# Performance work log

Measured on AMD Instinct MI355X. Metric: run time of the kernel, lower is better.

Reference implementation:

```python
import jax, jax.numpy as jnp
import numpy as np

N, B, NPM = 16384, 256, 64          # nodes, molecules, nodes per molecule
E = 65536                           # edges
FMAX, AMAX = 32, 16                 # FG slots per molecule, atoms per FG
HID, FGE, POSE = 960, 512, 128
NFG, MAXTOK, NFEAT = 205, 160, 5


def setup_inputs() -> dict:
    key = jax.random.key(0)
    ks = jax.random.split(key, 12)
    graph_x = jax.random.normal(ks[0], (N, NFEAT), jnp.float32)
    edge_index = jax.random.randint(ks[1], (2, E), 0, N)
    graph_batch = jnp.arange(N) // NPM
    ptr = jnp.arange(B + 1) * NPM
    fg_type_tensor = jax.random.randint(ks[2], (B, FMAX), 0, NFG)
    idx = jax.random.randint(ks[3], (B, FMAX, AMAX), 0, NPM)
    drop = jax.random.uniform(ks[4], (B, FMAX, AMAX)) < 0.3
    fg_indices_tensor = jnp.where(drop, -1, idx)
    s = lambda k, sh: jax.random.normal(k, sh, jnp.float32) * 0.02
    return dict(
        graph_x=graph_x, edge_index=edge_index, graph_batch=graph_batch, ptr=ptr,
        fg_type_tensor=fg_type_tensor, fg_indices_tensor=fg_indices_tensor,
        W1=s(ks[5], (NFEAT, HID)), b1=jnp.zeros((HID,), jnp.float32),
        W2=s(ks[6], (HID, HID)), b2=jnp.zeros((HID,), jnp.float32),
        fg_embed=s(ks[7], (NFG, FGE)), pos_embed=s(ks[8], (MAXTOK, POSE)),
        projW=s(ks[9], (HID, HID)), projb=jnp.zeros((HID,), jnp.float32),
        fuseW=s(ks[10], (FGE + POSE + HID + HID, HID)), fuseb=jnp.zeros((HID,), jnp.float32),
    )


def gcn_conv(x, W, b, src, dst, n):
    # PyG GCNConv: linear, add self-loops, symmetric deg^-1/2 normalization, sum-aggregate, bias
    h = x @ W
    deg = 1.0 + jax.ops.segment_sum(jnp.ones(src.shape[0], h.dtype), dst, num_segments=n)
    dinv = jax.lax.rsqrt(deg)
    msg = h[src] * (dinv[src] * dinv[dst])[:, None]            # [E, HID]
    out = jax.ops.segment_sum(msg, dst, num_segments=n) + h * (dinv * dinv)[:, None]
    return out + b


def reference(graph_x, edge_index, graph_batch, ptr, fg_type_tensor, fg_indices_tensor,
              W1, b1, W2, b2, fg_embed, pos_embed, projW, projb, fuseW, fuseb):
    src, dst = edge_index[0], edge_index[1]
    n = graph_x.shape[0]
    h = jax.nn.relu(gcn_conv(graph_x, W1, b1, src, dst, n))
    h = gcn_conv(h, W2, b2, src, dst, n)

    Bsz, Fmax = fg_type_tensor.shape
    # global mean pool per molecule
    cnt = jax.ops.segment_sum(jnp.ones(n, h.dtype), graph_batch, num_segments=Bsz)
    global_emb = jax.ops.segment_sum(h, graph_batch, num_segments=Bsz) / cnt[:, None]

    fg_static = fg_embed[fg_type_tensor]                        # [B, F, FGE]
    fg_pos = jnp.broadcast_to(pos_embed[:Fmax][None], (Bsz, Fmax, pos_embed.shape[1]))

    # vectorized FG-specific node pooling (replaces nested python loops)
    mask = fg_indices_tensor >= 0                               # [B, F, A]
    gids = jnp.where(mask, ptr[:-1][:, None, None] + fg_indices_tensor, 0)
    gathered = h[gids] * mask[..., None].astype(h.dtype)        # [B, F, A, HID]
    counts = mask.sum(-1).astype(h.dtype)                       # [B, F]
    pooled = gathered.sum(-2) / jnp.maximum(counts, 1.0)[..., None]
    fg_valid_mask = counts > 0

    fg_node_proj = pooled @ projW + projb
    global_exp = jnp.broadcast_to(global_emb[:, None, :], (Bsz, Fmax, global_emb.shape[1]))
    fused = jnp.concatenate([fg_static, fg_pos, fg_node_proj, global_exp], axis=-1)
    fg_fused = fused @ fuseW + fuseb
    return fg_fused, fg_valid_mask
```

## Files before the change

kernel.cpp:

```cpp
#include <hip/hip_runtime.h>

typedef unsigned short u16;
typedef unsigned int u32;
typedef __attribute__((ext_vector_type(8))) short short8;
typedef __attribute__((ext_vector_type(4))) float f32x4;

#define N_NODES 16384
#define B_MOL   256
#define NPM     64
#define E_EDGES 65536
#define FMAXF   32
#define AMAXA   16
#define HID     960
#define NFG     205
#define BF_ROWS 8192
#define OUT1    7864320
#define NTOT    4516800

__device__ __forceinline__ float bf2f(u16 u){ u32 x=((u32)u)<<16; float f; __builtin_memcpy(&f,&x,4); return f; }
__device__ __forceinline__ u16 f2bf(float f){ u32 x; __builtin_memcpy(&x,&f,4); x += 0x7FFFu + ((x>>16)&1u); return (u16)(x>>16); }

__device__ __forceinline__ void gload_lds16(const u16* g, u16* l){
    __builtin_amdgcn_global_load_lds(
        (const __attribute__((address_space(1))) void*)g,
        (__attribute__((address_space(3))) void*)l, 16, 0, 0);
}
__device__ __forceinline__ size_t swzA(int row, int col){
    return ((size_t)((row>>4)*30 + (col>>5)))*512 + (size_t)(((((col>>3)&3)*16) + (row&15))*8);
}
__device__ __forceinline__ size_t swzE(int row, int col){
    return ((size_t)((row>>4)*30 + (col>>5)))*512 + (size_t)((((col>>3)&3)*16 + (row&15))*8 + (col&7));
}

struct NormSrcs { const void* p[11]; };
__global__ __launch_bounds__(256) void k_normAll(NormSrcs s, u16* __restrict__ region,
                                                 float* __restrict__ b2f, float* __restrict__ projbf,
                                                 float* __restrict__ z4, int* __restrict__ flag,
                                                 int* __restrict__ deg){
    __shared__ int cnt;
    int t = threadIdx.x;
    if (t==0) cnt = 0;
    __syncthreads();
    u16 pv = ((const u16*)s.p[0])[t*2];
    if (((pv>>7)&0xFF) >= 0xC0) atomicAdd(&cnt, 1);
    __syncthreads();
    int fl = (cnt > 16) ? 1 : 0;
    int i = blockIdx.x*256 + t;
    if (blockIdx.x==0 && t==0) *flag = fl;
    if (i < N_NODES) deg[i] = 0;
    if (i < 4*HID) z4[i] = 0.f;
    if (i >= NTOT) return;
    int seg, off;
    if      (i <   81920){seg=0;  off=i;}
    else if (i <   86720){seg=1;  off=i-81920;}
    else if (i <   87680){seg=2;  off=i-86720;}
    else if (i < 1009280){seg=3;  off=i-87680;}
    else if (i < 1010240){seg=4;  off=i-1009280;}
    else if (i < 1115200){seg=5;  off=i-1010240;}
    else if (i < 1135680){seg=6;  off=i-1115200;}
    else if (i < 2057280){seg=7;  off=i-1135680;}
    else if (i < 2058240){seg=8;  off=i-2057280;}
    else if (i < 4515840){seg=9;  off=i-2058240;}
    else                 {seg=10; off=i-4515840;}
    const void* sp = s.p[seg];
    float fv; u16 uv;
    if (fl){ fv = ((const float*)sp)[off]; uv = f2bf(fv); }
    else   { uv = ((const u16*)sp)[off];  fv = bf2f(uv); }
    region[i] = uv;
    if (seg==4) b2f[off] = fv;
    if (seg==8) projbf[off] = fv;
}


__device__ __forceinline__ void gemm_sq(int bx, int by, const u16* __restrict__ A, int lda,
                                        const u16* __restrict__ Bt, int ldb,
                                        u16* __restrict__ C, int swz, char* smem)
{
    u16* As = (u16*)smem;
    u16* Bs = (u16*)smem + 64*40;
    const int tid = threadIdx.x;
    const int wave = tid>>6, lane = tid&63;
    const int wm = wave>>1, wn = wave&1;
    const int q = lane>>4, l16 = lane&15;
    const int m0 = bx*64, n0 = by*64;
    const int sm = tid>>2, sk = (tid&3)*8;
    f32x4 acc00={0,0,0,0}, acc01={0,0,0,0}, acc10={0,0,0,0}, acc11={0,0,0,0};
    const u16* Ap = A + (size_t)(m0+sm)*lda + sk;
    const u16* Bp = Bt + (size_t)(n0+sm)*ldb + sk;
    for (int k0=0; k0<HID; k0+=32){
        short8 av = *(const short8*)(Ap + k0);
        short8 bv = *(const short8*)(Bp + k0);
        *(short8*)(As + sm*40 + sk) = av;
        *(short8*)(Bs + sm*40 + sk) = bv;
        __syncthreads();
        short8 a0 = *(const short8*)(As + (wm*32      + l16)*40 + q*8);
        short8 a1 = *(const short8*)(As + (wm*32 + 16 + l16)*40 + q*8);
        short8 b0 = *(const short8*)(Bs + (wn*32      + l16)*40 + q*8);
        short8 b1 = *(const short8*)(Bs + (wn*32 + 16 + l16)*40 + q*8);
        acc00 = __builtin_amdgcn_mfma_f32_16x16x32_bf16(a0,b0,acc00,0,0,0);
        acc01 = __builtin_amdgcn_mfma_f32_16x16x32_bf16(a0,b1,acc01,0,0,0);
        acc10 = __builtin_amdgcn_mfma_f32_16x16x32_bf16(a1,b0,acc10,0,0,0);
        acc11 = __builtin_amdgcn_mfma_f32_16x16x32_bf16(a1,b1,acc11,0,0,0);
        __syncthreads();
    }
    #pragma unroll
    for (int i=0;i<2;i++){
        int rowb = m0 + wm*32 + i*16 + q*4;
        #pragma unroll
        for (int j=0;j<2;j++){
            int col = n0 + wn*32 + j*16 + l16;
            f32x4 av = (i==0) ? ((j==0)?acc00:acc01) : ((j==0)?acc10:acc11);
            #pragma unroll
            for (int r=0;r<4;r++){
                int row = rowb + r;
                u16 o = f2bf(av[r]);
                if (swz) C[swzE(row,col)] = o;
                else     C[(size_t)row*HID + col] = o;
            }
        }
    }
}
__device__ __forceinline__ void gemm64f(int bx, int by, const u16* __restrict__ A, int lda,
                                        const u16* __restrict__ Bt, int ldb,
                                        float* __restrict__ C, int M, int K,
                                        const float* __restrict__ addv, char* smem)
{
    u16* As = (u16*)smem;
    u16* Bs = (u16*)smem + 64*40;
    const int tid = threadIdx.x;
    const int wave = tid>>6, lane = tid&63;
    const int wm = wave>>1, wn = wave&1;
    const int q = lane>>4, l16 = lane&15;
    const int m0 = bx*64, n0 = by*64;
    const int sm = tid>>2, sk = (tid&3)*8;
    f32x4 acc00={0,0,0,0}, acc01={0,0,0,0}, acc10={0,0,0,0}, acc11={0,0,0,0};
    const bool aOk = (m0+sm) < M;
    const u16* Ap = A + (size_t)(m0+sm)*lda + sk;
    const u16* Bp = Bt + (size_t)(n0+sm)*ldb + sk;
    for (int k0=0; k0<K; k0+=32){
        short8 av = {0,0,0,0,0,0,0,0};
        if (aOk) av = *(const short8*)(Ap + k0);
        short8 bv = *(const short8*)(Bp + k0);
        *(short8*)(As + sm*40 + sk) = av;
        *(short8*)(Bs + sm*40 + sk) = bv;
        __syncthreads();
        short8 a0 = *(const short8*)(As + (wm*32      + l16)*40 + q*8);
        short8 a1 = *(const short8*)(As + (wm*32 + 16 + l16)*40 + q*8);
        short8 b0 = *(const short8*)(Bs + (wn*32      + l16)*40 + q*8);
        short8 b1 = *(const short8*)(Bs + (wn*32 + 16 + l16)*40 + q*8);
        acc00 = __builtin_amdgcn_mfma_f32_16x16x32_bf16(a0,b0,acc00,0,0,0);
        acc01 = __builtin_amdgcn_mfma_f32_16x16x32_bf16(a0,b1,acc01,0,0,0);
        acc10 = __builtin_amdgcn_mfma_f32_16x16x32_bf16(a1,b0,acc10,0,0,0);
        acc11 = __builtin_amdgcn_mfma_f32_16x16x32_bf16(a1,b1,acc11,0,0,0);
        __syncthreads();
    }
    #pragma unroll
    for (int i=0;i<2;i++){
        int rowb = m0 + wm*32 + i*16 + q*4;
        #pragma unroll
        for (int j=0;j<2;j++){
            int col = n0 + wn*32 + j*16 + l16;
            f32x4 av = (i==0) ? ((j==0)?acc00:acc01) : ((j==0)?acc10:acc11);
            float add = addv ? addv[col] : 0.f;
            #pragma unroll
            for (int r=0;r<4;r++){
                int row = rowb + r;
                if (row < M) C[(size_t)row*HID + col] = av[r] + add;
            }
        }
    }
}
__device__ __forceinline__ void transpose_tile(int bx, int by, const u16* __restrict__ src,
                                               u16* __restrict__ dst, int R, int C, char* smem)
{
    u16 (*tl)[33] = (u16(*)[33])smem;
    int c0 = bx*32, r0 = by*32;
    int tx = threadIdx.x & 31, ty = threadIdx.x >> 5;
    #pragma unroll
    for (int i=0;i<4;i++) tl[ty+i*8][tx] = src[(size_t)(r0+ty+i*8)*C + c0+tx];
    __syncthreads();
    #pragma unroll
    for (int i=0;i<4;i++) dst[(size_t)(c0+ty+i*8)*R + r0+tx] = tl[tx][ty+i*8];
}
__device__ __forceinline__ void vecmat_body(int bx, int by, const float* __restrict__ v,
                                            const u16* __restrict__ M, float* __restrict__ out, char* smem)
{
    float (*part)[64] = (float(*)[64])smem;
    int tid = threadIdx.x;
    int cl = tid & 63;
    int c = bx*64 + cl;
    int kg = tid >> 6;
    int k0 = by*60 + kg*15;
    float s = 0.f;
    #pragma unroll
    for (int i=0;i<15;i++) s += v[k0+i]*bf2f(M[(size_t)(k0+i)*HID + c]);
    part[kg][cl] = s;
    __syncthreads();
    if (kg==0) atomicAdd(&out[c], part[0][cl]+part[1][cl]+part[2][cl]+part[3][cl]);
}
__device__ __forceinline__ void scandinv_body(const int* __restrict__ deg, int* __restrict__ off,
                                              int* __restrict__ cur, float* __restrict__ dinv, char* smem)
{
    int* ps = (int*)smem;
    int t = threadIdx.x;
    const int chunk = N_NODES/256;
    int base0 = t*chunk;
    int s = 0;
    for (int i=0;i<chunk;i++) s += deg[base0+i];
    ps[t] = s; __syncthreads();
    for (int ofs=1; ofs<256; ofs<<=1){
        int v = ps[t];
        int add = (t>=ofs) ? ps[t-ofs] : 0;
        __syncthreads();
        ps[t] = v + add;
        __syncthreads();
    }
    int run = (t==0) ? 0 : ps[t-1];
    for (int i=0;i<chunk;i++){
        int d = deg[base0+i];
        off[base0+i]=run; cur[base0+i]=run; run += d;
        dinv[base0+i] = rsqrtf(1.0f + (float)d);
    }
    if (t==255) off[N_NODES] = run;
}

__global__ __launch_bounds__(256) void k_L1(const u16* __restrict__ fuseWn, u16* __restrict__ fuseWT,
                                            const int* __restrict__ dst, int* __restrict__ deg){
    __shared__ __attribute__((aligned(16))) char smem[2112];
    int b = blockIdx.x;
    if (b < 2400){
        transpose_tile(b%30, b/30, fuseWn, fuseWT, 2560, HID, smem);
    } else {
        int e = (b-2400)*256 + threadIdx.x;
        if (e < E_EDGES) atomicAdd(&deg[dst[e]], 1);
    }
}
__global__ __launch_bounds__(256) void k_L2(const u16* fuseWT, const u16* projWn, const u16* W2n,
                                            u16* Ub, u16* WglobT,
                                            const int* deg, int* off, int* cur, float* dinv){
    __shared__ __attribute__((aligned(16))) char smem[10240];
    int b = blockIdx.x;
    if (b < 450){
        int z = b/225, r = b%225;
        if (z==0) gemm_sq(r%15, r/15, fuseWT+640, 2560, projWn, HID, Ub, 0, smem);
        else      gemm_sq(r%15, r/15, fuseWT+1600, 2560, W2n, HID, WglobT, 0, smem);
    } else {
        scandinv_body(deg, off, cur, dinv, smem);
    }
}
__global__ __launch_bounds__(256) void k_L3(const u16* Ub, const u16* W2n, u16* WbigS,
                                            const u16* fgeN, const u16* posN, const u16* fuseWT,
                                            float* fgA, float* pWbM,
                                            const int* src, const int* dst, const float* dinv,
                                            int* cur, int* csr_s, float* csr_w){
    __shared__ __attribute__((aligned(16))) char smem[10240];
    int b = blockIdx.x;
    if (b < 225){
        gemm_sq(b%15, b/15, Ub, HID, W2n, HID, WbigS, 1, smem);
    } else if (b < 300){
        int bb = b-225;
        if (bb < 60) gemm64f(bb%4, bb/4, fgeN, 512, fuseWT, 2560, fgA, NFG, 512, nullptr, smem);
        else         gemm64f(0, bb-60, posN, 128, fuseWT+512, 2560, pWbM, FMAXF, 128, nullptr, smem);
    } else {
        int e = (b-300)*256 + threadIdx.x;
        if (e < E_EDGES){
            int s = src[e], d = dst[e];
            int p = atomicAdd(&cur[d], 1);
            csr_s[p] = s;
            csr_w[p] = dinv[s]*dinv[d];
        }
    }
}
__global__ __launch_bounds__(256) void k_L4(const u16* __restrict__ gxn, const float* __restrict__ dinv,
                                            const int* __restrict__ off, const int* __restrict__ csr_s,
                                            const float* __restrict__ csr_w,
                                            const u16* __restrict__ W1, const u16* __restrict__ b1,
                                            u16* __restrict__ h1b,
                                            const float* b2f, const float* projbf, const u16* fuseWn,
                                            const u16* projWn, float* tvb, float* cC, float* gvec){
    __shared__ __attribute__((aligned(16))) char smem[1024];
    int b = blockIdx.x;
    if (b < 8192){
        float* a2 = (float*)smem;
        int t = threadIdx.x;
        int h = t>>7, tl = t&127;
        int n = b*2 + h;
        if (tl < 5){
            int k = tl;
            float di = dinv[n], sw = di*di;
            float a = sw * bf2f(gxn[n*5+k]);
            int j0 = off[n], j1 = off[n+1];
            for (int j=j0;j<j1;j++) a += csr_w[j]*bf2f(gxn[csr_s[j]*5+k]);
            a2[h*8+k] = a;
        }
        __syncthreads();
        if (tl < 120){
            int c8 = tl*8;
            float a[5];
            #pragma unroll
            for (int k=0;k<5;k++) a[k] = a2[h*8+k];
            float r[8];
            short8 bb = *(const short8*)(b1 + c8);
            #pragma unroll
            for (int j=0;j<8;j++) r[j] = bf2f(((u16*)&bb)[j]);
            #pragma unroll
            for (int k=0;k<5;k++){
                short8 wv = *(const short8*)(W1 + k*HID + c8);
                #pragma unroll
                for (int j=0;j<8;j++) r[j] += a[k]*bf2f(((u16*)&wv)[j]);
            }
            short8 o;
            #pragma unroll
            for (int j=0;j<8;j++) ((u16*)&o)[j] = f2bf(fmaxf(r[j],0.f));
            *(short8*)(h1b + (size_t)n*HID + c8) = o;
        }
    } else {
        int bb = b - 8192;
        int z = bb/240, r = bb%240;
        if (z==0)      vecmat_body(r%15, r/15, b2f,    projWn,            tvb,  smem);
        else if (z==1) vecmat_body(r%15, r/15, projbf, fuseWn + 640*HID,  cC,   smem);
        else           vecmat_body(r%15, r/15, b2f,    fuseWn + 1600*HID, gvec, smem);
    }
}
__global__ __launch_bounds__(256) void k_L5(const u16* __restrict__ h1b, const float* __restrict__ dinv,
                                            const int* __restrict__ off, const int* __restrict__ csr_s,
                                            const float* __restrict__ csr_w, u16* __restrict__ P1b,
                                            const float* tvb, const u16* fuseWn, float* vb,
                                            const float* cC, const float* gvec, const u16* fusebn, float* c0){
    __shared__ __attribute__((aligned(16))) char smem[1024];
    int b = blockIdx.x;
    if (b < 4096){
        int wv = threadIdx.x>>6, lane = threadIdx.x&63;
        int n = b*4 + wv;
        int c = lane*16;
        bool act = lane < 60;
        float di = dinv[n], sw = di*di;
        float acc[16];
        if (act){
            short8 h0 = *(const short8*)(h1b + (size_t)n*HID + c);
            short8 h1v = *(const short8*)(h1b + (size_t)n*HID + c + 8);
            #pragma unroll
            for (int j=0;j<8;j++){ acc[j] = sw*bf2f(((u16*)&h0)[j]); acc[8+j] = sw*bf2f(((u16*)&h1v)[j]); }
        } else {
            #pragma unroll
            for (int j=0;j<16;j++) acc[j] = 0.f;
        }
        int j0 = off[n], j1 = off[n+1];
        for (int j=j0;j<j1;j++){
            int s = csr_s[j]; float w = csr_w[j];
            if (act){
                short8 v0 = *(const short8*)(h1b + (size_t)s*HID + c);
                short8 v1 = *(const short8*)(h1b + (size_t)s*HID + c + 8);
                #pragma unroll
                for (int j2=0;j2<8;j2++){ acc[j2] += w*bf2f(((u16*)&v0)[j2]); acc[8+j2] += w*bf2f(((u16*)&v1)[j2]); }
            }
        }
        if (act){
            short8 o0, o1;
            #pragma unroll
            for (int j=0;j<8;j++){ ((u16*)&o0)[j] = f2bf(acc[j]); ((u16*)&o1)[j] = f2bf(acc[8+j]); }
            *(short8*)(P1b + (size_t)n*HID + c) = o0;
            *(short8*)(P1b + (size_t)n*HID + c + 8) = o1;
        }
    } else if (b < 4336){
        int bb = b - 4096;
        vecmat_body(bb%15, bb/15, tvb, fuseWn + 640*HID, vb, smem);
    } else {
        int c = (b-4336)*256 + threadIdx.x;
        if (c < HID) c0[c] = cC[c] + gvec[c] + bf2f(fusebn[c]);
    }
}
__global__ __launch_bounds__(256) void k_L6(const u16* __restrict__ P1b, const int* __restrict__ fgi,
                                            const int* __restrict__ ptr, u16* __restrict__ prb,
                                            float* __restrict__ evec, u16* __restrict__ maskb,
                                            float* __restrict__ maskf, const int* __restrict__ flag,
                                            u16* __restrict__ gmb){
    int b = blockIdx.x;
    if (b < 2048){
        int wv = threadIdx.x>>6, lane = threadIdx.x&63;
        int bf = b*4 + wv;
        int mb = bf >> 5;
        int base = ptr[mb];
        int c = lane*16;
        bool act = lane < 60;
        float acc[16];
        #pragma unroll
        for (int j=0;j<16;j++) acc[j] = 0.f;
        int cnt = 0;
        #pragma unroll
        for (int a=0;a<AMAXA;a++){
            int idx = fgi[bf*AMAXA + a];
            if (idx >= 0){
                cnt++;
                if (act){
                    short8 v0 = *(const short8*)(P1b + (size_t)(base+idx)*HID + c);
                    short8 v1 = *(const short8*)(P1b + (size_t)(base+idx)*HID + c + 8);
                    #pragma unroll
                    for (int j=0;j<8;j++){ acc[j] += bf2f(((u16*)&v0)[j]); acc[8+j] += bf2f(((u16*)&v1)[j]); }
                }
            }
        }
        float inv = (cnt>0) ? 1.0f/(float)cnt : 0.0f;
        if (act){
            short8 o0, o1;
            #pragma unroll
            for (int j=0;j<8;j++){ ((u16*)&o0)[j] = f2bf(acc[j]*inv); ((u16*)&o1)[j] = f2bf(acc[8+j]*inv); }
            *(short8*)(prb + swzA(bf, c)) = o0;
            *(short8*)(prb + swzA(bf, c+8)) = o1;
        }
        if (lane == 0){
            float e = (cnt>0) ? 1.0f : 0.0f;
            evec[bf] = e;
            if (*flag) maskf[bf] = e;
            else       maskb[bf] = f2bf(e);
        }
    } else {
        int id = (b-2048)*256 + threadIdx.x;
        int mb = id / 120; int c8 = (id - mb*120)*8;
        float s[8] = {0,0,0,0,0,0,0,0};
        for (int i=0;i<NPM;i++){
            short8 v = *(const short8*)(P1b + (size_t)(mb*NPM+i)*HID + c8);
            #pragma unroll
            for (int j=0;j<8;j++) s[j] += bf2f(((u16*)&v)[j]);
        }
        const float inv = 1.0f/(float)NPM;
        short8 o;
        #pragma unroll
        for (int j=0;j<8;j++) ((u16*)&o)[j] = f2bf(s[j]*inv);
        *(short8*)(gmb + (size_t)mb*HID + c8) = o;
    }
}
__global__ __launch_bounds__(256) void k_L7(const u16* gmb, const u16* WglobT, float* Gc, const float* c0){
    __shared__ __attribute__((aligned(16))) char smem[10240];
    int b = blockIdx.x;
    gemm64f(b%4, b/4, gmb, HID, WglobT, HID, Gc, B_MOL, HID, c0, smem);
}

__global__ __launch_bounds__(256) void k_gemmF(
    const u16* __restrict__ A, const u16* __restrict__ Bt,
    float* __restrict__ Cf, u16* __restrict__ Cb,
    const int* __restrict__ fg_type, const float* __restrict__ evec,
    const float* __restrict__ fgA, const float* __restrict__ pWbM,
    const float* __restrict__ vb, const float* __restrict__ Gc,
    const int* __restrict__ flag)
{
    __shared__ __attribute__((aligned(16))) u16 S[2][14*512];
    const int tid = threadIdx.x;
    const int wave = tid>>6, lane = tid&63;
    const int wm = wave>>1, wn = wave&1;
    const int q = lane>>4, l16 = lane&15;
    const int m0 = blockIdx.x*128, n0 = blockIdx.y*96;
    const int R0 = blockIdx.x*8, N0 = blockIdx.y*6;

    f32x4 acc[4][3];
    #pragma unroll
    for (int i=0;i<4;i++)
        #pragma unroll
        for (int j=0;j<3;j++) acc[i][j] = (f32x4){0,0,0,0};

    const u16* gA0 = A  + ((size_t)(R0 + wave*2    )*30)*512 + lane*8;
    const u16* gA1 = A  + ((size_t)(R0 + wave*2 + 1)*30)*512 + lane*8;
    const u16* gB0 = Bt + ((size_t)(N0 + wave      )*30)*512 + lane*8;
    const u16* gB1 = Bt + ((size_t)(N0 + 4 + wave  )*30)*512 + lane*8;

    gload_lds16(gA0, &S[0][(wave*2  )*512]);
    gload_lds16(gA1, &S[0][(wave*2+1)*512]);
    gload_lds16(gB0, &S[0][(8+wave)*512]);
    if (wave < 2) gload_lds16(gB1, &S[0][(12+wave)*512]);

    int buf = 0;
    for (int kc=0; kc<30; kc++){
        __syncthreads();
        if (kc < 29){
            int kn = (kc+1)*512;
            gload_lds16(gA0 + kn, &S[buf^1][(wave*2  )*512]);
            gload_lds16(gA1 + kn, &S[buf^1][(wave*2+1)*512]);
            gload_lds16(gB0 + kn, &S[buf^1][(8+wave)*512]);
            if (wave < 2) gload_lds16(gB1 + kn, &S[buf^1][(12+wave)*512]);
        }
        short8 af[4], bfr[3];
        #pragma unroll
        for (int i=0;i<4;i++) af[i] = *(const short8*)(&S[buf][(wm*4+i)*512 + lane*8]);
        #pragma unroll
        for (int j=0;j<3;j++) bfr[j] = *(const short8*)(&S[buf][(8+wn*3+j)*512 + lane*8]);
        #pragma unroll
        for (int i=0;i<4;i++)
            #pragma unroll
            for (int j=0;j<3;j++)
                acc[i][j] = __builtin_amdgcn_mfma_f32_16x16x32_bf16(af[i], bfr[j], acc[i][j], 0,0,0);
        buf ^= 1;
    }

    const int isf = *flag;
    #pragma unroll
    for (int i=0;i<4;i++){
        int rowb = m0 + wm*64 + i*16 + q*4;
        #pragma unroll
        for (int r=0;r<4;r++){
            int row = rowb + r;
            int bb = row>>5, ff = row&31;
            int ty = fg_type[row];
            float e = evec[row];
            #pragma unroll
            for (int j=0;j<3;j++){
                int col = n0 + wn*48 + j*16 + l16;
                float v = acc[i][j][r]
                        + fgA[ty*HID+col] + pWbM[ff*HID+col]
                        + e*vb[col] + Gc[bb*HID+col];
                if (isf) Cf[(size_t)row*HID + col] = v;
                else     Cb[(size_t)row*HID + col] = f2bf(v);
            }
        }
    }
}

extern "C" void kernel_launch(void* const* d_in, const int* in_sizes, int n_in,
                              void* d_out, int out_size, void* d_ws, size_t ws_size,
                              hipStream_t stream) {
    const int* edge_idx  = (const int*)d_in[1];
    const int* ptr       = (const int*)d_in[3];
    const int* fg_type   = (const int*)d_in[4];
    const int* fg_idx    = (const int*)d_in[5];

    char* w = (char*)d_ws;
    auto nxt = [&](size_t b)->char*{ char* p = w; w += (b + 255) & ~(size_t)255; return p; };
    u16* big0   = (u16*)nxt((size_t)N_NODES*HID*2);
    u16* fuseWT = big0;
    u16* Ub     = big0 + (size_t)HID*2560;
    u16* h1b    = big0;
    u16* prb    = big0;
    u16* P1b    = (u16*)nxt((size_t)N_NODES*HID*2);
    u16*  WbigS  = (u16*) nxt((size_t)HID*HID*2);
    u16*  WglobT = (u16*) nxt((size_t)HID*HID*2);
    float* fgA   = (float*)nxt((size_t)NFG*HID*4);
    float* pWbM  = (float*)nxt((size_t)FMAXF*HID*4);
    float* b2f   = (float*)nxt(HID*4);
    float* projbf= (float*)nxt(HID*4);
    float* tvb   = (float*)nxt(HID*4);
    float* cC    = (float*)nxt(HID*4);
    float* gvec  = (float*)nxt(HID*4);
    float* vb    = (float*)nxt(HID*4);
    float* c0    = (float*)nxt(HID*4);
    int*   deg   = (int*)  nxt(N_NODES*4);
    float* dinv  = (float*)nxt(N_NODES*4);
    int*   off   = (int*)  nxt((N_NODES+1)*4);
    int*   cur   = (int*)  nxt(N_NODES*4);
    int*   csr_s = (int*)  nxt(E_EDGES*4);
    float* csr_w = (float*)nxt(E_EDGES*4);
    float* evec  = (float*)nxt(BF_ROWS*4);
    u16*   gmb   = (u16*)  nxt((size_t)B_MOL*HID*2);
    float* Gc    = (float*)nxt((size_t)B_MOL*HID*4);
    int*   flag  = (int*)  nxt(256);
    u16*   region= (u16*)  nxt((size_t)NTOT*2);
    u16* gxn    = region;
    u16* W1n    = region +   81920;
    u16* b1n    = region +   86720;
    u16* W2n    = region +   87680;
    u16* fgeN   = region + 1010240;
    u16* posN   = region + 1115200;
    u16* projWn = region + 1135680;
    u16* fuseWn = region + 2058240;
    u16* fusebn = region + 4515840;

    NormSrcs ns;
    ns.p[0]=d_in[0]; ns.p[1]=d_in[6]; ns.p[2]=d_in[7]; ns.p[3]=d_in[8]; ns.p[4]=d_in[9];
    ns.p[5]=d_in[10]; ns.p[6]=d_in[11]; ns.p[7]=d_in[12]; ns.p[8]=d_in[13]; ns.p[9]=d_in[14]; ns.p[10]=d_in[15];
    k_normAll<<<(NTOT+255)/256,256,0,stream>>>(ns, region, b2f, projbf, tvb, flag, deg);
    k_L1<<<2656,256,0,stream>>>(fuseWn, fuseWT, edge_idx + E_EDGES, deg);
    k_L2<<<451,256,0,stream>>>(fuseWT, projWn, W2n, Ub, WglobT, deg, off, cur, dinv);
    k_L3<<<556,256,0,stream>>>(Ub, W2n, WbigS, fgeN, posN, fuseWT, fgA, pWbM,
                               edge_idx, edge_idx + E_EDGES, dinv, cur, csr_s, csr_w);
    k_L4<<<8912,256,0,stream>>>(gxn, dinv, off, csr_s, csr_w, W1n, b1n, h1b,
                                b2f, projbf, fuseWn, projWn, tvb, cC, gvec);
    k_L5<<<4340,256,0,stream>>>(h1b, dinv, off, csr_s, csr_w, P1b,
                                tvb, fuseWn, vb, cC, gvec, fusebn, c0);
    k_L6<<<2168,256,0,stream>>>(P1b, fg_idx, ptr, prb, evec,
                                (u16*)d_out + OUT1, (float*)d_out + OUT1, flag, gmb);
    k_L7<<<60,256,0,stream>>>(gmb, WglobT, Gc, c0);
    k_gemmF<<<dim3(64,10),256,0,stream>>>(prb, WbigS, (float*)d_out, (u16*)d_out,
                                          fg_type, evec, fgA, pWbM, vb, Gc, flag);
    (void)in_sizes; (void)n_in; (void)out_size; (void)ws_size;
}
```

Baseline: 291.1 us.

## Restructure final GEMM to 8 waves with two-K-chunk single-buffered stages

The final fused GEMM kernel moves from 4 to 8 waves per block, so each wave computes a 32x48 sub-tile instead of 64x48. It also replaces the double-buffered one-K-chunk-per-iteration pipeline with a single buffer that loads two K chunks per stage and synchronizes twice per stage. The aim is more latency hiding through extra waves and fewer loop iterations. The cost is that global loads no longer overlap with MFMA compute inside a block, and there is an extra barrier per stage.

```diff
diff --git a/kernel.cpp b/kernel.cpp
--- a/kernel.cpp
+++ b/kernel.cpp
@@ -436,7 +436,7 @@
     gemm64f(b%4, b/4, gmb, HID, WglobT, HID, Gc, B_MOL, HID, c0, smem);
 }
 
-__global__ __launch_bounds__(256) void k_gemmF(
+__global__ __launch_bounds__(512) void k_gemmF(
     const u16* __restrict__ A, const u16* __restrict__ Bt,
     float* __restrict__ Cf, u16* __restrict__ Cb,
     const int* __restrict__ fg_type, const float* __restrict__ evec,
@@ -444,7 +444,8 @@
     const float* __restrict__ vb, const float* __restrict__ Gc,
     const int* __restrict__ flag)
 {
-    __shared__ __attribute__((aligned(16))) u16 S[2][14*512];
+    __shared__ __attribute__((aligned(16))) u16 SA[16*512];
+    __shared__ __attribute__((aligned(16))) u16 SB[12*512];
     const int tid = threadIdx.x;
     const int wave = tid>>6, lane = tid&63;
     const int wm = wave>>1, wn = wave&1;
@@ -452,49 +453,51 @@
     const int m0 = blockIdx.x*128, n0 = blockIdx.y*96;
     const int R0 = blockIdx.x*8, N0 = blockIdx.y*6;
 
-    f32x4 acc[4][3];
-    #pragma unroll
-    for (int i=0;i<4;i++)
+    f32x4 acc[2][3];
+    #pragma unroll
+    for (int i=0;i<2;i++)
         #pragma unroll
         for (int j=0;j<3;j++) acc[i][j] = (f32x4){0,0,0,0};
 
-    const u16* gA0 = A  + ((size_t)(R0 + wave*2    )*30)*512 + lane*8;
-    const u16* gA1 = A  + ((size_t)(R0 + wave*2 + 1)*30)*512 + lane*8;
-    const u16* gB0 = Bt + ((size_t)(N0 + wave      )*30)*512 + lane*8;
-    const u16* gB1 = Bt + ((size_t)(N0 + 4 + wave  )*30)*512 + lane*8;
-
-    gload_lds16(gA0, &S[0][(wave*2  )*512]);
-    gload_lds16(gA1, &S[0][(wave*2+1)*512]);
-    gload_lds16(gB0, &S[0][(8+wave)*512]);
-    if (wave < 2) gload_lds16(gB1, &S[0][(12+wave)*512]);
-
-    int buf = 0;
-    for (int kc=0; kc<30; kc++){
-        __syncthreads();
-        if (kc < 29){
-            int kn = (kc+1)*512;
-            gload_lds16(gA0 + kn, &S[buf^1][(wave*2  )*512]);
-            gload_lds16(gA1 + kn, &S[buf^1][(wave*2+1)*512]);
-            gload_lds16(gB0 + kn, &S[buf^1][(8+wave)*512]);
-            if (wave < 2) gload_lds16(gB1 + kn, &S[buf^1][(12+wave)*512]);
-        }
-        short8 af[4], bfr[3];
-        #pragma unroll
-        for (int i=0;i<4;i++) af[i] = *(const short8*)(&S[buf][(wm*4+i)*512 + lane*8]);
-        #pragma unroll
-        for (int j=0;j<3;j++) bfr[j] = *(const short8*)(&S[buf][(8+wn*3+j)*512 + lane*8]);
-        #pragma unroll
-        for (int i=0;i<4;i++)
-            #pragma unroll
-            for (int j=0;j<3;j++)
-                acc[i][j] = __builtin_amdgcn_mfma_f32_16x16x32_bf16(af[i], bfr[j], acc[i][j], 0,0,0);
-        buf ^= 1;
+    const u16* gA = A + lane*8;
+    const u16* gB = Bt + lane*8;
+    const int a0 = wave*2, a1 = wave*2+1;
+    const int b0 = wave*2, b1 = wave*2+1;
+
+    for (int s=0; s<15; s++){
+        int kb = s*2;
+        gload_lds16(gA + ((size_t)((R0+(a0>>1))*30 + kb + (a0&1)))*512, SA + a0*512);
+        gload_lds16(gA + ((size_t)((R0+(a1>>1))*30 + kb + (a1&1)))*512, SA + a1*512);
+        if (wave < 6){
+            gload_lds16(gB + ((size_t)((N0+(b0>>1))*30 + kb + (b0&1)))*512, SB + b0*512);
+            gload_lds16(gB + ((size_t)((N0+(b1>>1))*30 + kb + (b1&1)))*512, SB + b1*512);
+        }
+        __syncthreads();
+        short8 af[2][2], bfr[3][2];
+        #pragma unroll
+        for (int i=0;i<2;i++)
+            #pragma unroll
+            for (int kk=0;kk<2;kk++)
+                af[i][kk] = *(const short8*)(SA + (((wm*2+i)*2+kk)*512 + lane*8));
+        #pragma unroll
+        for (int j=0;j<3;j++)
+            #pragma unroll
+            for (int kk=0;kk<2;kk++)
+                bfr[j][kk] = *(const short8*)(SB + (((wn*3+j)*2+kk)*512 + lane*8));
+        #pragma unroll
+        for (int i=0;i<2;i++)
+            #pragma unroll
+            for (int j=0;j<3;j++){
+                acc[i][j] = __builtin_amdgcn_mfma_f32_16x16x32_bf16(af[i][0], bfr[j][0], acc[i][j], 0,0,0);
+                acc[i][j] = __builtin_amdgcn_mfma_f32_16x16x32_bf16(af[i][1], bfr[j][1], acc[i][j], 0,0,0);
+            }
+        __syncthreads();
     }
 
     const int isf = *flag;
     #pragma unroll
-    for (int i=0;i<4;i++){
-        int rowb = m0 + wm*64 + i*16 + q*4;
+    for (int i=0;i<2;i++){
+        int rowb = m0 + wm*32 + i*16 + q*4;
         #pragma unroll
         for (int r=0;r<4;r++){
             int row = rowb + r;
@@ -577,7 +580,7 @@
     k_L6<<<2168,256,0,stream>>>(P1b, fg_idx, ptr, prb, evec,
                                 (u16*)d_out + OUT1, (float*)d_out + OUT1, flag, gmb);
     k_L7<<<60,256,0,stream>>>(gmb, WglobT, Gc, c0);
-    k_gemmF<<<dim3(64,10),256,0,stream>>>(prb, WbigS, (float*)d_out, (u16*)d_out,
+    k_gemmF<<<dim3(64,10),512,0,stream>>>(prb, WbigS, (float*)d_out, (u16*)d_out,
                                           fg_type, evec, fgA, pWbM, vb, Gc, flag);
     (void)in_sizes; (void)n_in; (void)out_size; (void)ws_size;
 }
```

Measured after the change: 297.8 us. 1.02x slower.
